# Kernel tuning notes

Measured on AMD Instinct MI355X. Metric: run time of the kernel, lower is better.

## Reference

```python
import jax, jax.numpy as jnp
import numpy as np


def setup_inputs() -> dict:
    key = jax.random.key(0)
    k_x, k_w, k_b = jax.random.split(key, 3)
    B, F, D, H = 4096, 64, 128, 4
    inputs = jax.random.normal(k_x, (B, F, D), dtype=jnp.float32)
    w = jax.random.normal(k_w, (H, D), dtype=jnp.float32)
    b = jax.random.normal(k_b, (H,), dtype=jnp.float32)
    return {"inputs": inputs, "w": w, "b": b}


def reference(inputs, w, b):
    # pairwise outer-product contracted with head weights:
    # scores[b,i,j,h] = sum_d x[b,i,d] * x[b,j,d] * w[h,d]
    scores = jnp.einsum('bid,bjd,hd->bijh', inputs, inputs, w) + b  # [B,F,F,H]
    s = jnp.sum(scores, axis=-1)  # [B,F,F]
    denom = jnp.sum(s, axis=(1, 2), keepdims=True)  # [B,1,1]
    return s / denom
```

## Files before the change

### kernel.cpp

```cpp
#include <hip/hip_runtime.h>
#include <hip/hip_bf16.h>


constexpr int F = 64;
constexpr int D = 128;

using bf16x8 = __attribute__((ext_vector_type(8))) short;
using f32x4  = __attribute__((ext_vector_type(4))) float;

__device__ __forceinline__ unsigned pk2(float lo, float hi) {
    float2 f2; f2.x = lo; f2.y = hi;
    __hip_bfloat162 h = __float22bfloat162_rn(f2);
    union { __hip_bfloat162 h2; unsigned u; } cv; cv.h2 = h;
    return cv.u;
}

__global__ __launch_bounds__(256, 4) void afm_kernel(
    const float* __restrict__ x, const float* __restrict__ w,
    const float* __restrict__ bias, float* __restrict__ out)
{
    __shared__ float sX[F * D];
    __shared__ float sW[D];
    __shared__ float sSp[8][D];

    const int t      = threadIdx.x;
    const int blk    = blockIdx.x;
    const int lane   = t & 63;
    const int wv     = t >> 6;
    const int l31    = lane & 31;
    const int rowpar = t >> 5;

    if (t < D) sW[t] = w[t] + w[D + t] + w[2 * D + t] + w[3 * D + t];
    const float bsum = bias[0] + bias[1] + bias[2] + bias[3];

    const float* xb = x + (size_t)blk * (F * D);
    const int cb = l31 ^ rowpar;
    const float* srcbase = xb + rowpar * D + cb * 4;
    #pragma unroll
    for (int k = 0; k < 8; ++k) {
        const float* src = srcbase + k * 8 * D;
        float* dst = sX + (k * 4 + wv) * 256;
        __builtin_amdgcn_global_load_lds(
            (const __attribute__((address_space(1))) void*)src,
            (__attribute__((address_space(3))) void*)dst,
            16, 0, 0);
    }
    __syncthreads();

    float4 c4 = {0.f, 0.f, 0.f, 0.f};
    #pragma unroll
    for (int k = 0; k < 8; ++k) {
        const float4 v = *reinterpret_cast<const float4*>(sX + (k * 4 + wv) * 256 + lane * 4);
        c4.x += v.x; c4.y += v.y; c4.z += v.z; c4.w += v.w;
    }
    *reinterpret_cast<float4*>(&sSp[rowpar][4 * cb]) = c4;
    __syncthreads();

    float S0 = 0.f, S1 = 0.f;
    #pragma unroll
    for (int p8 = 0; p8 < 8; ++p8) { S0 += sSp[p8][lane]; S1 += sSp[p8][64 + lane]; }
    float dp = S0 * S0 * sW[lane] + S1 * S1 * sW[64 + lane];
    #pragma unroll
    for (int off = 32; off; off >>= 1) dp += __shfl_xor(dp, off, 64);
    const float rden = 1.0f / (dp + 4096.0f * bsum);

    f32x4 acc[4] = {{0,0,0,0},{0,0,0,0},{0,0,0,0},{0,0,0,0}};
    const int fr   = lane & 15;
    const int kgrp = lane >> 4;
    const int r_a  = wv * 16 + fr;
    const char* sXc = reinterpret_cast<const char*>(sX);
    const int rowA = r_a * 512;
    const int swA  = (r_a & 7) << 4;
    const int swB  = (fr & 7) << 4;

    #pragma unroll
    for (int s = 0; s < 4; ++s) {
        const int ch    = 4 * s + kgrp;
        const int cbyte = ch * 32;
        const int aA = rowA + (cbyte ^ swA);
        const float4 a0 = *reinterpret_cast<const float4*>(sXc + aA);
        const float4 a1 = *reinterpret_cast<const float4*>(sXc + (aA ^ 16));
        const float4 wa = *reinterpret_cast<const float4*>(&sW[ch * 8]);
        const float4 wb = *reinterpret_cast<const float4*>(&sW[ch * 8 + 4]);
        union { uint4 u; bf16x8 v; } af;
        af.u.x = pk2(a0.x * wa.x, a0.y * wa.y);
        af.u.y = pk2(a0.z * wa.z, a0.w * wa.w);
        af.u.z = pk2(a1.x * wb.x, a1.y * wb.y);
        af.u.w = pk2(a1.z * wb.z, a1.w * wb.w);
        #pragma unroll
        for (int tj = 0; tj < 4; ++tj) {
            const int aB = (tj * 16 + fr) * 512 + (cbyte ^ swB);
            const float4 b0 = *reinterpret_cast<const float4*>(sXc + aB);
            const float4 b1 = *reinterpret_cast<const float4*>(sXc + (aB ^ 16));
            union { uint4 u; bf16x8 v; } bf;
            bf.u.x = pk2(b0.x, b0.y); bf.u.y = pk2(b0.z, b0.w);
            bf.u.z = pk2(b1.x, b1.y); bf.u.w = pk2(b1.z, b1.w);
            acc[tj] = __builtin_amdgcn_mfma_f32_16x16x32_bf16(af.v, bf.v, acc[tj], 0, 0, 0);
        }
    }

    const int rbase = wv * 16 + 4 * kgrp;
    float* ob = out + (size_t)blk * (F * F);
    #pragma unroll
    for (int tj = 0; tj < 4; ++tj) {
        float4 o;
        o.x = (acc[tj][0] + bsum) * rden;
        o.y = (acc[tj][1] + bsum) * rden;
        o.z = (acc[tj][2] + bsum) * rden;
        o.w = (acc[tj][3] + bsum) * rden;
        *reinterpret_cast<float4*>(ob + (size_t)(tj * 16 + fr) * F + rbase) = o;
    }
}

extern "C" void kernel_launch(void* const* d_in, const int* in_sizes, int n_in,
                              void* d_out, int out_size, void* d_ws, size_t ws_size,
                              hipStream_t stream) {
    const float* x  = (const float*)d_in[0];
    const float* w  = (const float*)d_in[1];
    const float* b  = (const float*)d_in[2];
    float* out      = (float*)d_out;

    afm_kernel<<<4096, 256, 0, stream>>>(x, w, b, out);
}
```

Measured before the change: 37.00 us.

## Process eight batches per block with double-buffered LDS prefetch

Each block now handles eight consecutive batch elements instead of one, so the grid shrinks from 4096 to 512 blocks. The next batch's tile is prefetched into a second LDS buffer with global_load_lds while the current one is reduced and multiplied with MFMA. The aim is to hide global-load latency behind compute and to amortise per-block setup such as the weight sum. In exchange, LDS per block roughly doubles and launch bounds drop to two blocks per CU. That lowers resident occupancy and the number of memory requests in flight, and each iteration's trailing vmcnt(0) wait also waits on the output stores.

```diff
diff --git a/kernel.cpp b/kernel.cpp
--- a/kernel.cpp
+++ b/kernel.cpp
@@ -15,16 +15,15 @@
     return cv.u;
 }
 
-__global__ __launch_bounds__(256, 4) void afm_kernel(
+__global__ __launch_bounds__(256, 2) void afm_kernel(
     const float* __restrict__ x, const float* __restrict__ w,
     const float* __restrict__ bias, float* __restrict__ out)
 {
-    __shared__ float sX[F * D];
+    __shared__ float sX[2][F * D];
     __shared__ float sW[D];
     __shared__ float sSp[8][D];
 
     const int t      = threadIdx.x;
-    const int blk    = blockIdx.x;
     const int lane   = t & 63;
     const int wv     = t >> 6;
     const int l31    = lane & 31;
@@ -33,82 +32,96 @@
     if (t < D) sW[t] = w[t] + w[D + t] + w[2 * D + t] + w[3 * D + t];
     const float bsum = bias[0] + bias[1] + bias[2] + bias[3];
 
-    const float* xb = x + (size_t)blk * (F * D);
+    const size_t b0 = (size_t)blockIdx.x * 8;
+    const float* xb = x + b0 * (F * D);
     const int cb = l31 ^ rowpar;
     const float* srcbase = xb + rowpar * D + cb * 4;
-    #pragma unroll
-    for (int k = 0; k < 8; ++k) {
-        const float* src = srcbase + k * 8 * D;
-        float* dst = sX + (k * 4 + wv) * 256;
-        __builtin_amdgcn_global_load_lds(
-            (const __attribute__((address_space(1))) void*)src,
-            (__attribute__((address_space(3))) void*)dst,
-            16, 0, 0);
-    }
-    __syncthreads();
 
-    float4 c4 = {0.f, 0.f, 0.f, 0.f};
-    #pragma unroll
-    for (int k = 0; k < 8; ++k) {
-        const float4 v = *reinterpret_cast<const float4*>(sX + (k * 4 + wv) * 256 + lane * 4);
-        c4.x += v.x; c4.y += v.y; c4.z += v.z; c4.w += v.w;
-    }
-    *reinterpret_cast<float4*>(&sSp[rowpar][4 * cb]) = c4;
-    __syncthreads();
+    auto STAGE = [&](int buf, int m) {
+        const float* sb = srcbase + (size_t)m * (F * D);
+        #pragma unroll
+        for (int k = 0; k < 8; ++k) {
+            __builtin_amdgcn_global_load_lds(
+                (const __attribute__((address_space(1))) void*)(sb + k * 8 * D),
+                (__attribute__((address_space(3))) void*)(&sX[buf][(k * 4 + wv) * 256]),
+                16, 0, 0);
+        }
+    };
 
-    float S0 = 0.f, S1 = 0.f;
-    #pragma unroll
-    for (int p8 = 0; p8 < 8; ++p8) { S0 += sSp[p8][lane]; S1 += sSp[p8][64 + lane]; }
-    float dp = S0 * S0 * sW[lane] + S1 * S1 * sW[64 + lane];
-    #pragma unroll
-    for (int off = 32; off; off >>= 1) dp += __shfl_xor(dp, off, 64);
-    const float rden = 1.0f / (dp + 4096.0f * bsum);
+    STAGE(0, 0);
+    asm volatile("s_waitcnt vmcnt(0) lgkmcnt(0)\n\ts_barrier" ::: "memory");
 
-    f32x4 acc[4] = {{0,0,0,0},{0,0,0,0},{0,0,0,0},{0,0,0,0}};
-    const int fr   = lane & 15;
-    const int kgrp = lane >> 4;
-    const int r_a  = wv * 16 + fr;
-    const char* sXc = reinterpret_cast<const char*>(sX);
-    const int rowA = r_a * 512;
-    const int swA  = (r_a & 7) << 4;
-    const int swB  = (fr & 7) << 4;
+    const int fr    = lane & 15;
+    const int kgrp  = lane >> 4;
+    const int r_a   = wv * 16 + fr;
+    const int rowA  = r_a * 512;
+    const int swA   = (r_a & 7) << 4;
+    const int swB   = (fr & 7) << 4;
+    const int rbase = wv * 16 + 4 * kgrp;
 
-    #pragma unroll
-    for (int s = 0; s < 4; ++s) {
-        const int ch    = 4 * s + kgrp;
-        const int cbyte = ch * 32;
-        const int aA = rowA + (cbyte ^ swA);
-        const float4 a0 = *reinterpret_cast<const float4*>(sXc + aA);
-        const float4 a1 = *reinterpret_cast<const float4*>(sXc + (aA ^ 16));
-        const float4 wa = *reinterpret_cast<const float4*>(&sW[ch * 8]);
-        const float4 wb = *reinterpret_cast<const float4*>(&sW[ch * 8 + 4]);
-        union { uint4 u; bf16x8 v; } af;
-        af.u.x = pk2(a0.x * wa.x, a0.y * wa.y);
-        af.u.y = pk2(a0.z * wa.z, a0.w * wa.w);
-        af.u.z = pk2(a1.x * wb.x, a1.y * wb.y);
-        af.u.w = pk2(a1.z * wb.z, a1.w * wb.w);
+    #pragma unroll 2
+    for (int m = 0; m < 8; ++m) {
+        const int cur = m & 1;
+        if (m < 7) STAGE(cur ^ 1, m + 1);
+
+        const char* sXc = reinterpret_cast<const char*>(&sX[cur][0]);
+
+        float4 c4 = {0.f, 0.f, 0.f, 0.f};
+        #pragma unroll
+        for (int k = 0; k < 8; ++k) {
+            const float4 v = *reinterpret_cast<const float4*>(&sX[cur][(k * 4 + wv) * 256 + lane * 4]);
+            c4.x += v.x; c4.y += v.y; c4.z += v.z; c4.w += v.w;
+        }
+        *reinterpret_cast<float4*>(&sSp[rowpar][4 * cb]) = c4;
+        asm volatile("s_waitcnt lgkmcnt(0)\n\ts_barrier" ::: "memory");
+
+        float S0 = 0.f, S1 = 0.f;
+        #pragma unroll
+        for (int p8 = 0; p8 < 8; ++p8) { S0 += sSp[p8][lane]; S1 += sSp[p8][64 + lane]; }
+        float dp = S0 * S0 * sW[lane] + S1 * S1 * sW[64 + lane];
+        #pragma unroll
+        for (int off = 32; off; off >>= 1) dp += __shfl_xor(dp, off, 64);
+        const float rden = 1.0f / (dp + 4096.0f * bsum);
+
+        f32x4 acc[4] = {{0,0,0,0},{0,0,0,0},{0,0,0,0},{0,0,0,0}};
+        #pragma unroll
+        for (int s = 0; s < 4; ++s) {
+            const int ch    = 4 * s + kgrp;
+            const int cbyte = ch * 32;
+            const int aA = rowA + (cbyte ^ swA);
+            const float4 a0 = *reinterpret_cast<const float4*>(sXc + aA);
+            const float4 a1 = *reinterpret_cast<const float4*>(sXc + (aA ^ 16));
+            const float4 wa = *reinterpret_cast<const float4*>(&sW[ch * 8]);
+            const float4 wb = *reinterpret_cast<const float4*>(&sW[ch * 8 + 4]);
+            union { uint4 u; bf16x8 v; } af;
+            af.u.x = pk2(a0.x * wa.x, a0.y * wa.y);
+            af.u.y = pk2(a0.z * wa.z, a0.w * wa.w);
+            af.u.z = pk2(a1.x * wb.x, a1.y * wb.y);
+            af.u.w = pk2(a1.z * wb.z, a1.w * wb.w);
+            #pragma unroll
+            for (int tj = 0; tj < 4; ++tj) {
+                const int aB = (tj * 16 + fr) * 512 + (cbyte ^ swB);
+                const float4 bv0 = *reinterpret_cast<const float4*>(sXc + aB);
+                const float4 bv1 = *reinterpret_cast<const float4*>(sXc + (aB ^ 16));
+                union { uint4 u; bf16x8 v; } bf;
+                bf.u.x = pk2(bv0.x, bv0.y); bf.u.y = pk2(bv0.z, bv0.w);
+                bf.u.z = pk2(bv1.x, bv1.y); bf.u.w = pk2(bv1.z, bv1.w);
+                acc[tj] = __builtin_amdgcn_mfma_f32_16x16x32_bf16(af.v, bf.v, acc[tj], 0, 0, 0);
+            }
+        }
+
+        float* ob = out + (b0 + m) * (size_t)(F * F);
         #pragma unroll
         for (int tj = 0; tj < 4; ++tj) {
-            const int aB = (tj * 16 + fr) * 512 + (cbyte ^ swB);
-            const float4 b0 = *reinterpret_cast<const float4*>(sXc + aB);
-            const float4 b1 = *reinterpret_cast<const float4*>(sXc + (aB ^ 16));
-            union { uint4 u; bf16x8 v; } bf;
-            bf.u.x = pk2(b0.x, b0.y); bf.u.y = pk2(b0.z, b0.w);
-            bf.u.z = pk2(b1.x, b1.y); bf.u.w = pk2(b1.z, b1.w);
-            acc[tj] = __builtin_amdgcn_mfma_f32_16x16x32_bf16(af.v, bf.v, acc[tj], 0, 0, 0);
+            float4 o;
+            o.x = (acc[tj][0] + bsum) * rden;
+            o.y = (acc[tj][1] + bsum) * rden;
+            o.z = (acc[tj][2] + bsum) * rden;
+            o.w = (acc[tj][3] + bsum) * rden;
+            *reinterpret_cast<float4*>(ob + (size_t)(tj * 16 + fr) * F + rbase) = o;
         }
-    }
 
-    const int rbase = wv * 16 + 4 * kgrp;
-    float* ob = out + (size_t)blk * (F * F);
-    #pragma unroll
-    for (int tj = 0; tj < 4; ++tj) {
-        float4 o;
-        o.x = (acc[tj][0] + bsum) * rden;
-        o.y = (acc[tj][1] + bsum) * rden;
-        o.z = (acc[tj][2] + bsum) * rden;
-        o.w = (acc[tj][3] + bsum) * rden;
-        *reinterpret_cast<float4*>(ob + (size_t)(tj * 16 + fr) * F + rbase) = o;
+        asm volatile("s_waitcnt vmcnt(0)\n\ts_barrier" ::: "memory");
     }
 }
 
@@ -120,5 +133,5 @@
     const float* b  = (const float*)d_in[2];
     float* out      = (float*)d_out;
 
-    afm_kernel<<<4096, 256, 0, stream>>>(x, w, b, out);
+    afm_kernel<<<512, 256, 0, stream>>>(x, w, b, out);
 }
```

Result: slower. 41.13 us (+11.2%).
